# Kernel tuning notes

Hardware: AMD Instinct MI355X
Metric: run time of the kernel (lower is better)

The kernel has to match this reference:

```python
import jax, jax.numpy as jnp
import numpy as np

# ---- static config matching init_kwargs ----
B, H, S, D = 1, 16, 8192, 64
BS = 64                  # block_size (= block_m = block_n here)
NB = S // BS             # 128 query/key blocks
LOCAL = 8                # local window width in blocks

# Block-level sparse pattern: causal, global block 0 + local window of 8 blocks.
_pat = np.zeros((NB, NB), dtype=bool)
for _i in range(NB):
    _pat[_i, 0] = True
    _pat[_i, max(0, _i - LOCAL + 1):_i + 1] = True
MAX_NNZ = int(_pat.sum(1).max())  # 9
_cols = np.zeros((NB, MAX_NNZ), np.int32)
_cmask = np.zeros((NB, MAX_NNZ), bool)
for _i in range(NB):
    _nz = np.nonzero(_pat[_i])[0]
    _cols[_i, :len(_nz)] = _nz
    _cmask[_i, :len(_nz)] = True
COLS = jnp.asarray(_cols)        # [NB, MAX_NNZ] padded column block indices
COLMASK = jnp.asarray(_cmask)    # [NB, MAX_NNZ] validity of padded entries
NEG_INF = jnp.float32(-1e30)


def setup_inputs() -> dict:
    key = jax.random.key(0)
    kq, kk, kv = jax.random.split(key, 3)
    q = jax.random.normal(kq, (B, H, S, D), dtype=jnp.float32)
    k = jax.random.normal(kk, (B, H, S, D), dtype=jnp.float32)
    v = jax.random.normal(kv, (B, H, S, D), dtype=jnp.float32)
    return {"q": q, "k": k, "v": v}


def reference(q, k, v):
    sm_scale = 1.0 / float(np.sqrt(D))
    qb = q.reshape(B, H, NB, BS, D)
    kb = k.reshape(B, H, NB, BS, D)
    vb = v.reshape(B, H, NB, BS, D)
    # gather only the nonzero key/value blocks per query block (honor sparsity)
    kg = kb[:, :, COLS]  # [B,H,NB,MAX_NNZ,BS,D]
    vg = vb[:, :, COLS]  # [B,H,NB,MAX_NNZ,BS,D]
    scores = jnp.einsum('bhimd,bhinjd->bhimnj', qb, kg) * sm_scale  # [B,H,NB,BS,MAX_NNZ,BS]
    # causal + padded-block mask
    q_pos = jnp.arange(NB, dtype=jnp.int32)[:, None] * BS + jnp.arange(BS, dtype=jnp.int32)[None, :]   # [NB,BS]
    k_pos = COLS[:, :, None] * BS + jnp.arange(BS, dtype=jnp.int32)                                     # [NB,MAX_NNZ,BS]
    mask = (k_pos[:, None, :, :] <= q_pos[:, :, None, None]) & COLMASK[:, None, :, None]                # [NB,BS,MAX_NNZ,BS]
    scores = jnp.where(mask, scores, NEG_INF)
    p = jax.nn.softmax(scores.reshape(B, H, NB, BS, MAX_NNZ * BS), axis=-1)
    out = jnp.einsum('bhimn,bhind->bhimd', p, vg.reshape(B, H, NB, MAX_NNZ * BS, D))
    return out.reshape(B, H, S, D)
```

## Files before the change

kernel.cpp:

```cpp
#include <hip/hip_runtime.h>
#include <hip/hip_bf16.h>
#include <string.h>

typedef __attribute__((ext_vector_type(8))) short short8;
typedef __attribute__((ext_vector_type(4))) float floatx4;

#define HH 16
#define SS 8192
#define DD 64
#define NBQ 128
#define NTILE (HH * NBQ)
#define TILE_ELEMS 4096
#define LOG2E 1.44269504088896f
#define WS_NEEDED ((size_t)NTILE * TILE_ELEMS * 2 * 2)

__device__ __forceinline__ unsigned pkbf(float a, float b) {
    __hip_bfloat162 h2 = __float22bfloat162_rn(make_float2(a, b));
    unsigned r;
    memcpy(&r, &h2, 4);
    return r;
}

__device__ __forceinline__ void gload16(const void* g, void* l) {
    __builtin_amdgcn_global_load_lds(
        (const __attribute__((address_space(1))) unsigned int*)g,
        (__attribute__((address_space(3))) unsigned int*)l, 16, 0, 0);
}

__device__ __forceinline__ float red_sum4(float x) {
    x += __shfl_xor(x, 16);
    return x + __shfl_xor(x, 32);
}

__global__ __launch_bounds__(256, 4) void prep_kernel(
        const float* __restrict__ kg, const float* __restrict__ vg,
        unsigned short* __restrict__ kimg, unsigned short* __restrict__ vtimg) {
    __shared__ float lv[64 * 64];
    const int tile = (int)blockIdx.x;
    const int tid = (int)threadIdx.x;
    const float* kb = kg + (size_t)tile * TILE_ELEMS;
    const float* vb = vg + (size_t)tile * TILE_ELEMS;
    unsigned short* ko = kimg + (size_t)tile * TILE_ELEMS;
    unsigned short* vo = vtimg + (size_t)tile * TILE_ELEMS;

    const int row = tid >> 2;
    const int c16 = (tid & 3) * 16;

    {
        const float* src = kb + row * 64 + c16;
        float4 a = ((const float4*)src)[0];
        float4 b = ((const float4*)src)[1];
        float4 c = ((const float4*)src)[2];
        float4 d = ((const float4*)src)[3];
        uint4 lo, hi;
        lo.x = pkbf(a.x, a.y); lo.y = pkbf(a.z, a.w);
        lo.z = pkbf(b.x, b.y); lo.w = pkbf(b.z, b.w);
        hi.x = pkbf(c.x, c.y); hi.y = pkbf(c.z, c.w);
        hi.z = pkbf(d.x, d.y); hi.w = pkbf(d.z, d.w);
        const int sw = (row & 7) << 3;
        *(uint4*)(ko + row * 64 + (c16 ^ sw)) = lo;
        *(uint4*)(ko + row * 64 + ((c16 + 8) ^ sw)) = hi;
    }

    {
        const float4* src = (const float4*)(vb + row * 64 + c16);
        float4* dst = (float4*)(&lv[row * 64 + c16]);
        dst[0] = src[0]; dst[1] = src[1]; dst[2] = src[2]; dst[3] = src[3];
    }
    __syncthreads();
    {
        const int d = row;
        const int kc16 = c16;
        float x[16];
        #pragma unroll
        for (int kk = 0; kk < 16; ++kk) x[kk] = lv[(kc16 + kk) * 64 + d];
        const int sw = (d & 7) << 3;
        const int rot = (d & 15) << 2;
        #pragma unroll
        for (int q4 = 0; q4 < 4; ++q4) {
            uint2 pk;
            pk.x = pkbf(x[4 * q4], x[4 * q4 + 1]);
            pk.y = pkbf(x[4 * q4 + 2], x[4 * q4 + 3]);
            const int c = (((kc16 + 4 * q4) ^ sw) + rot) & 63;
            *(uint2*)(vo + d * 64 + c) = pk;
        }
    }
}

__global__ __launch_bounds__(256, 4) void sparse_attn_kernel(
        const float* __restrict__ qg, const unsigned short* __restrict__ kimg,
        const unsigned short* __restrict__ vtimg, float* __restrict__ og) {
    __shared__ unsigned short lds_k[2][TILE_ELEMS];
    __shared__ unsigned short lds_vt[2][TILE_ELEMS];

    const int bid = (int)blockIdx.x;
    const int work = (bid & 7) * 256 + (bid >> 3);
    const int h = work >> 7;
    const int i = work & (NBQ - 1);
    const int tid = (int)threadIdx.x;
    const int w = tid >> 6;
    const int lane = tid & 63;
    const int lp = lane & 15;
    const int g = lane >> 4;

    const unsigned short* ktiles = kimg + (size_t)h * NBQ * TILE_ELEMS;
    const unsigned short* vtiles = vtimg + (size_t)h * NBQ * TILE_ELEMS;

    short8 qf[2];
    {
        const float sc = 0.125f * LOG2E;
        const float* qrow = qg + ((size_t)h * SS + i * 64 + w * 16 + lp) * DD;
        #pragma unroll
        for (int f = 0; f < 2; ++f) {
            const float* p0 = qrow + f * 32 + 8 * g;
            float4 x = *(const float4*)(p0);
            float4 y = *(const float4*)(p0 + 4);
            union { unsigned u[4]; short8 s; } t_;
            t_.u[0] = pkbf(x.x * sc, x.y * sc);
            t_.u[1] = pkbf(x.z * sc, x.w * sc);
            t_.u[2] = pkbf(y.x * sc, y.y * sc);
            t_.u[3] = pkbf(y.z * sc, y.w * sc);
            qf[f] = t_.s;
        }
    }

    floatx4 acc[4];
    #pragma unroll
    for (int tt = 0; tt < 4; ++tt) acc[tt] = (floatx4)(0.f);
    float lsum = 0.f;

    const int nnz = (i < 8) ? (i + 1) : 9;
    const int lane8 = lane * 8;

    auto stage = [&](int j, int b) {
        const unsigned short* ks = ktiles + (size_t)j * TILE_ELEMS + w * 512 + lane8;
        const unsigned short* vs = vtiles + (size_t)j * TILE_ELEMS + w * 512 + lane8;
        gload16(ks,        &lds_k[b][w * 512]);
        gload16(ks + 2048, &lds_k[b][2048 + w * 512]);
        gload16(vs,        &lds_vt[b][w * 512]);
        gload16(vs + 2048, &lds_vt[b][2048 + w * 512]);
    };

    stage(0, 0);
    __syncthreads();

    const int swl = (lp & 7) << 3;
    int vcol[4];
    #pragma unroll
    for (int r = 0; r < 4; ++r)
        vcol[r] = (((4 * g + 16 * r) ^ swl) + (lp << 2)) & 63;

    for (int t = 0; t < nnz; ++t) {
        const int j = (i < 8) ? t : ((t == 0) ? 0 : (i - 8 + t));
        const int buf = t & 1;

        if (t + 1 < nnz) {
            const int jn = (i < 8) ? (t + 1) : (i - 8 + (t + 1));
            stage(jn, buf ^ 1);
        }

        floatx4 st[4];
        #pragma unroll
        for (int kc = 0; kc < 4; ++kc) st[kc] = (floatx4)(0.f);
        #pragma unroll
        for (int kc = 0; kc < 4; ++kc) {
            const int row = kc * 16 + lp;
            const short8 kf0 = *(const short8*)(&lds_k[buf][row * 64 + ((8 * g) ^ swl)]);
            const short8 kf1 = *(const short8*)(&lds_k[buf][row * 64 + ((32 + 8 * g) ^ swl)]);
            st[kc] = __builtin_amdgcn_mfma_f32_16x16x32_bf16(kf0, qf[0], st[kc], 0, 0, 0);
            st[kc] = __builtin_amdgcn_mfma_f32_16x16x32_bf16(kf1, qf[1], st[kc], 0, 0, 0);
        }

        if (j == i) {
            #pragma unroll
            for (int kc = 0; kc < 4; ++kc) {
                #pragma unroll
                for (int r = 0; r < 4; ++r) {
                    const int key = kc * 16 + 4 * g + r;
                    if (key > w * 16 + lp) st[kc][r] = -1e30f;
                }
            }
        }

        #pragma unroll
        for (int kc = 0; kc < 4; ++kc) {
            #pragma unroll
            for (int r = 0; r < 4; ++r) {
                const float p = exp2f(st[kc][r]);
                st[kc][r] = p;
                lsum += p;
            }
        }

        union { unsigned u[4]; short8 s; } pf0_, pf1_;
        pf0_.u[0] = pkbf(st[0][0], st[0][1]); pf0_.u[1] = pkbf(st[0][2], st[0][3]);
        pf0_.u[2] = pkbf(st[1][0], st[1][1]); pf0_.u[3] = pkbf(st[1][2], st[1][3]);
        pf1_.u[0] = pkbf(st[2][0], st[2][1]); pf1_.u[1] = pkbf(st[2][2], st[2][3]);
        pf1_.u[2] = pkbf(st[3][0], st[3][1]); pf1_.u[3] = pkbf(st[3][2], st[3][3]);
        const short8 pf0 = pf0_.s;
        const short8 pf1 = pf1_.s;

        #pragma unroll
        for (int tt = 0; tt < 4; ++tt) {
            const unsigned short* vr = &lds_vt[buf][(tt * 16 + lp) * 64];
            union { uint2 p[2]; short8 s; } v0_, v1_;
            v0_.p[0] = *(const uint2*)(vr + vcol[0]);
            v0_.p[1] = *(const uint2*)(vr + vcol[1]);
            v1_.p[0] = *(const uint2*)(vr + vcol[2]);
            v1_.p[1] = *(const uint2*)(vr + vcol[3]);
            acc[tt] = __builtin_amdgcn_mfma_f32_16x16x32_bf16(v0_.s, pf0, acc[tt], 0, 0, 0);
            acc[tt] = __builtin_amdgcn_mfma_f32_16x16x32_bf16(v1_.s, pf1, acc[tt], 0, 0, 0);
        }

        if (t + 1 < nnz) __syncthreads();
    }

    const float rn = 1.0f / red_sum4(lsum);
    float* ob = og + ((size_t)h * SS + i * 64 + w * 16 + lp) * DD;
    #pragma unroll
    for (int tt = 0; tt < 4; ++tt) {
        float4 o4;
        o4.x = acc[tt][0] * rn;
        o4.y = acc[tt][1] * rn;
        o4.z = acc[tt][2] * rn;
        o4.w = acc[tt][3] * rn;
        *(float4*)(ob + tt * 16 + 4 * g) = o4;
    }
}

__global__ __launch_bounds__(256, 4) void sparse_attn_fb(
        const float* __restrict__ qg, const float* __restrict__ kg,
        const float* __restrict__ vg, float* __restrict__ og) {
    __shared__ unsigned short lds_k[2][64 * 64];
    __shared__ unsigned short lds_vt[2][64 * 64];
    __shared__ unsigned short lds_p[4][16 * 64];

    const int bid = (int)blockIdx.x;
    const int work = (bid & 7) * 256 + (bid >> 3);
    const int h = work >> 7;
    const int i = work & (NBQ - 1);
    const int tid = (int)threadIdx.x;
    const int w = tid >> 6;
    const int lane = tid & 63;
    const int lp = lane & 15;
    const int g = lane >> 4;

    const float* kh = kg + (size_t)h * SS * DD;
    const float* vh = vg + (size_t)h * SS * DD;

    short8 qf[2];
    {
        const float sc = 0.125f * LOG2E;
        const float* qrow = qg + ((size_t)h * SS + i * 64 + w * 16 + lp) * DD;
        #pragma unroll
        for (int f = 0; f < 2; ++f) {
            const float* p0 = qrow + f * 32 + 8 * g;
            float4 x = *(const float4*)(p0);
            float4 y = *(const float4*)(p0 + 4);
            union { unsigned u[4]; short8 s; } t_;
            t_.u[0] = pkbf(x.x * sc, x.y * sc);
            t_.u[1] = pkbf(x.z * sc, x.w * sc);
            t_.u[2] = pkbf(y.x * sc, y.y * sc);
            t_.u[3] = pkbf(y.z * sc, y.w * sc);
            qf[f] = t_.s;
        }
    }

    floatx4 acc[4];
    #pragma unroll
    for (int tt = 0; tt < 4; ++tt) acc[tt] = (floatx4)(0.f);
    float m = -1e30f;
    float lsum = 0.f;
    const int nnz = (i < 8) ? (i + 1) : 9;

    float4 kreg[4];
    float vreg[16];
    const int krow_sub = tid >> 4;
    const int kc4 = (tid & 15) * 4;

    {
        #pragma unroll
        for (int p = 0; p < 4; ++p)
            kreg[p] = *(const float4*)(kh + (p * 16 + krow_sub) * DD + kc4);
        #pragma unroll
        for (int kk = 0; kk < 16; ++kk)
            vreg[kk] = vh[(w * 16 + kk) * DD + lane];
    }

    const int swl = (lp & 7) << 3;

    for (int t = 0; t < nnz; ++t) {
        const int j = (i < 8) ? t : ((t == 0) ? 0 : (i - 8 + t));
        const int buf = t & 1;

        #pragma unroll
        for (int p = 0; p < 4; ++p) {
            const int row = p * 16 + krow_sub;
            uint2 pk;
            pk.x = pkbf(kreg[p].x, kreg[p].y);
            pk.y = pkbf(kreg[p].z, kreg[p].w);
            *(uint2*)(&lds_k[buf][row * 64 + (kc4 ^ ((row & 7) << 3))]) = pk;
        }
        {
            const int d = lane;
            const int sw = (d & 7) << 3;
            uint4 A, Bv;
            A.x = pkbf(vreg[0], vreg[1]);   A.y = pkbf(vreg[2], vreg[3]);
            A.z = pkbf(vreg[4], vreg[5]);   A.w = pkbf(vreg[6], vreg[7]);
            Bv.x = pkbf(vreg[8], vreg[9]);  Bv.y = pkbf(vreg[10], vreg[11]);
            Bv.z = pkbf(vreg[12], vreg[13]); Bv.w = pkbf(vreg[14], vreg[15]);
            *(uint4*)(&lds_vt[buf][d * 64 + ((w * 16) ^ sw)]) = A;
            *(uint4*)(&lds_vt[buf][d * 64 + ((w * 16 + 8) ^ sw)]) = Bv;
        }

        if (t + 1 < nnz) {
            const int jn = (i < 8) ? (t + 1) : (i - 8 + (t + 1));
            const float* kb = kh + jn * (64 * DD);
            const float* vb = vh + jn * (64 * DD);
            #pragma unroll
            for (int p = 0; p < 4; ++p)
                kreg[p] = *(const float4*)(kb + (p * 16 + krow_sub) * DD + kc4);
            #pragma unroll
            for (int kk = 0; kk < 16; ++kk)
                vreg[kk] = vb[(w * 16 + kk) * DD + lane];
        }

        __syncthreads();

        floatx4 st[4];
        #pragma unroll
        for (int kc = 0; kc < 4; ++kc) st[kc] = (floatx4)(0.f);
        #pragma unroll
        for (int kc = 0; kc < 4; ++kc) {
            const int row = kc * 16 + lp;
            const short8 kf0 = *(const short8*)(&lds_k[buf][row * 64 + ((8 * g) ^ swl)]);
            const short8 kf1 = *(const short8*)(&lds_k[buf][row * 64 + ((32 + 8 * g) ^ swl)]);
            st[kc] = __builtin_amdgcn_mfma_f32_16x16x32_bf16(kf0, qf[0], st[kc], 0, 0, 0);
            st[kc] = __builtin_amdgcn_mfma_f32_16x16x32_bf16(kf1, qf[1], st[kc], 0, 0, 0);
        }

        if (j == i) {
            #pragma unroll
            for (int kc = 0; kc < 4; ++kc) {
                #pragma unroll
                for (int r = 0; r < 4; ++r) {
                    const int key = kc * 16 + 4 * g + r;
                    if (key > w * 16 + lp) st[kc][r] = -1e30f;
                }
            }
        }

        float vmax = -1e30f;
        #pragma unroll
        for (int kc = 0; kc < 4; ++kc) {
            #pragma unroll
            for (int r = 0; r < 4; ++r) vmax = fmaxf(vmax, st[kc][r]);
        }
        vmax = fmaxf(vmax, __shfl_xor(vmax, 16));
        vmax = fmaxf(vmax, __shfl_xor(vmax, 32));
        const float m_new = fmaxf(m, vmax);
        const float alpha = exp2f(m - m_new);
        float psum = 0.f;
        #pragma unroll
        for (int kc = 0; kc < 4; ++kc) {
            #pragma unroll
            for (int r = 0; r < 4; ++r) {
                const float p = exp2f(st[kc][r] - m_new);
                st[kc][r] = p;
                psum += p;
            }
        }
        psum += __shfl_xor(psum, 16);
        psum += __shfl_xor(psum, 32);
        lsum = lsum * alpha + psum;
        m = m_new;
        #pragma unroll
        for (int tt = 0; tt < 4; ++tt) acc[tt] *= alpha;

        unsigned short* pw = lds_p[w];
        #pragma unroll
        for (int kc = 0; kc < 4; ++kc) {
            uint2 pk;
            pk.x = pkbf(st[kc][0], st[kc][1]);
            pk.y = pkbf(st[kc][2], st[kc][3]);
            const int e = lp * 64 + ((kc * 16 + 4 * g) ^ swl);
            *(uint2*)(&pw[e]) = pk;
        }

        const short8 pf0 = *(const short8*)(&pw[lp * 64 + ((8 * g) ^ swl)]);
        const short8 pf1 = *(const short8*)(&pw[lp * 64 + ((32 + 8 * g) ^ swl)]);
        #pragma unroll
        for (int tt = 0; tt < 4; ++tt) {
            const int row = tt * 16 + lp;
            const short8 vf0 = *(const short8*)(&lds_vt[buf][row * 64 + ((8 * g) ^ swl)]);
            const short8 vf1 = *(const short8*)(&lds_vt[buf][row * 64 + ((32 + 8 * g) ^ swl)]);
            acc[tt] = __builtin_amdgcn_mfma_f32_16x16x32_bf16(vf0, pf0, acc[tt], 0, 0, 0);
            acc[tt] = __builtin_amdgcn_mfma_f32_16x16x32_bf16(vf1, pf1, acc[tt], 0, 0, 0);
        }
    }

    const float rn = 1.0f / lsum;
    float* ob = og + ((size_t)h * SS + i * 64 + w * 16 + lp) * DD;
    #pragma unroll
    for (int tt = 0; tt < 4; ++tt) {
        float4 o4;
        o4.x = acc[tt][0] * rn;
        o4.y = acc[tt][1] * rn;
        o4.z = acc[tt][2] * rn;
        o4.w = acc[tt][3] * rn;
        *(float4*)(ob + tt * 16 + 4 * g) = o4;
    }
}

extern "C" void kernel_launch(void* const* d_in, const int* in_sizes, int n_in,
                              void* d_out, int out_size, void* d_ws, size_t ws_size,
                              hipStream_t stream) {
    const float* q = (const float*)d_in[0];
    const float* k = (const float*)d_in[1];
    const float* v = (const float*)d_in[2];
    float* out = (float*)d_out;

    if (ws_size >= WS_NEEDED) {
        unsigned short* kimg = (unsigned short*)d_ws;
        unsigned short* vtimg = kimg + (size_t)NTILE * TILE_ELEMS;
        prep_kernel<<<dim3(NTILE), dim3(256), 0, stream>>>(k, v, kimg, vtimg);
        sparse_attn_kernel<<<dim3(HH * NBQ), dim3(256), 0, stream>>>(q, kimg, vtimg, out);
    } else {
        sparse_attn_fb<<<dim3(HH * NBQ), dim3(256), 0, stream>>>(q, k, v, out);
    }
}
```

Measured before the change: 64.14 us.

## Process two adjacent query blocks per workgroup sharing K/V tile loads

Each workgroup now handles a pair of adjacent query blocks, iterating over the union of their key blocks (global block 0 plus the local window) and reusing each staged K/V tile for both queries. This removes the near-duplicate K/V loads that neighbouring query blocks made into LDS. In exchange the grid is halved to 1024 workgroups, register use roughly doubles for accumulators and scores, and per-tile branches skip MFMAs for blocks outside one query's window.

```diff
diff --git a/kernel.cpp b/kernel.cpp
--- a/kernel.cpp
+++ b/kernel.cpp
@@ -94,6 +94,209 @@
     __shared__ unsigned short lds_vt[2][TILE_ELEMS];
 
     const int bid = (int)blockIdx.x;
+    const int work = (bid & 7) * 128 + (bid >> 3);
+    const int h = work >> 6;
+    const int wi = work & 63;
+    const int i0 = 2 * wi;
+    const int i1 = i0 + 1;
+    const int tid = (int)threadIdx.x;
+    const int w = tid >> 6;
+    const int lane = tid & 63;
+    const int lp = lane & 15;
+    const int g = lane >> 4;
+
+    const unsigned short* ktiles = kimg + (size_t)h * NBQ * TILE_ELEMS;
+    const unsigned short* vtiles = vtimg + (size_t)h * NBQ * TILE_ELEMS;
+
+    short8 qfA[2], qfB[2];
+    {
+        const float sc = 0.125f * LOG2E;
+        const float* qrowA = qg + ((size_t)h * SS + i0 * 64 + w * 16 + lp) * DD;
+        const float* qrowB = qrowA + 64 * DD;
+        #pragma unroll
+        for (int f = 0; f < 2; ++f) {
+            const float* pA = qrowA + f * 32 + 8 * g;
+            float4 xa = *(const float4*)(pA);
+            float4 ya = *(const float4*)(pA + 4);
+            union { unsigned u[4]; short8 s; } tA;
+            tA.u[0] = pkbf(xa.x * sc, xa.y * sc);
+            tA.u[1] = pkbf(xa.z * sc, xa.w * sc);
+            tA.u[2] = pkbf(ya.x * sc, ya.y * sc);
+            tA.u[3] = pkbf(ya.z * sc, ya.w * sc);
+            qfA[f] = tA.s;
+            const float* pB = qrowB + f * 32 + 8 * g;
+            float4 xb = *(const float4*)(pB);
+            float4 yb = *(const float4*)(pB + 4);
+            union { unsigned u[4]; short8 s; } tB;
+            tB.u[0] = pkbf(xb.x * sc, xb.y * sc);
+            tB.u[1] = pkbf(xb.z * sc, xb.w * sc);
+            tB.u[2] = pkbf(yb.x * sc, yb.y * sc);
+            tB.u[3] = pkbf(yb.z * sc, yb.w * sc);
+            qfB[f] = tB.s;
+        }
+    }
+
+    floatx4 accA[4], accB[4];
+    #pragma unroll
+    for (int tt = 0; tt < 4; ++tt) { accA[tt] = (floatx4)(0.f); accB[tt] = (floatx4)(0.f); }
+    float lsumA = 0.f, lsumB = 0.f;
+
+    const int lo = (i0 < 8) ? 1 : (i0 - 7);
+    const int nt = i1 - lo + 2;
+    const int lane8 = lane * 8;
+
+    auto stage = [&](int j, int b) {
+        const unsigned short* ks = ktiles + (size_t)j * TILE_ELEMS + w * 512 + lane8;
+        const unsigned short* vs = vtiles + (size_t)j * TILE_ELEMS + w * 512 + lane8;
+        gload16(ks,        &lds_k[b][w * 512]);
+        gload16(ks + 2048, &lds_k[b][2048 + w * 512]);
+        gload16(vs,        &lds_vt[b][w * 512]);
+        gload16(vs + 2048, &lds_vt[b][2048 + w * 512]);
+    };
+
+    stage(0, 0);
+    __syncthreads();
+
+    const int swl = (lp & 7) << 3;
+    int vcol[4];
+    #pragma unroll
+    for (int r = 0; r < 4; ++r)
+        vcol[r] = (((4 * g + 16 * r) ^ swl) + (lp << 2)) & 63;
+
+    for (int t = 0; t < nt; ++t) {
+        const int j = (t == 0) ? 0 : (lo + t - 1);
+        const int buf = t & 1;
+
+        if (t + 1 < nt) stage(lo + t, buf ^ 1);
+
+        const bool cA = (j == 0) || (j >= i0 - 7 && j <= i0);
+        const bool cB = (j == 0) || (j >= i1 - 7 && j <= i1);
+
+        floatx4 stA[4], stB[4];
+        #pragma unroll
+        for (int kc = 0; kc < 4; ++kc) { stA[kc] = (floatx4)(0.f); stB[kc] = (floatx4)(0.f); }
+        #pragma unroll
+        for (int kc = 0; kc < 4; ++kc) {
+            const int row = kc * 16 + lp;
+            const short8 kf0 = *(const short8*)(&lds_k[buf][row * 64 + ((8 * g) ^ swl)]);
+            const short8 kf1 = *(const short8*)(&lds_k[buf][row * 64 + ((32 + 8 * g) ^ swl)]);
+            if (cA) {
+                stA[kc] = __builtin_amdgcn_mfma_f32_16x16x32_bf16(kf0, qfA[0], stA[kc], 0, 0, 0);
+                stA[kc] = __builtin_amdgcn_mfma_f32_16x16x32_bf16(kf1, qfA[1], stA[kc], 0, 0, 0);
+            }
+            if (cB) {
+                stB[kc] = __builtin_amdgcn_mfma_f32_16x16x32_bf16(kf0, qfB[0], stB[kc], 0, 0, 0);
+                stB[kc] = __builtin_amdgcn_mfma_f32_16x16x32_bf16(kf1, qfB[1], stB[kc], 0, 0, 0);
+            }
+        }
+
+        if (j == i0) {
+            #pragma unroll
+            for (int kc = 0; kc < 4; ++kc)
+                #pragma unroll
+                for (int r = 0; r < 4; ++r)
+                    if (kc * 16 + 4 * g + r > w * 16 + lp) stA[kc][r] = -1e30f;
+        }
+        if (j == i1) {
+            #pragma unroll
+            for (int kc = 0; kc < 4; ++kc)
+                #pragma unroll
+                for (int r = 0; r < 4; ++r)
+                    if (kc * 16 + 4 * g + r > w * 16 + lp) stB[kc][r] = -1e30f;
+        }
+
+        if (cA) {
+            #pragma unroll
+            for (int kc = 0; kc < 4; ++kc)
+                #pragma unroll
+                for (int r = 0; r < 4; ++r) {
+                    const float p = exp2f(stA[kc][r]);
+                    stA[kc][r] = p;
+                    lsumA += p;
+                }
+        }
+        if (cB) {
+            #pragma unroll
+            for (int kc = 0; kc < 4; ++kc)
+                #pragma unroll
+                for (int r = 0; r < 4; ++r) {
+                    const float p = exp2f(stB[kc][r]);
+                    stB[kc][r] = p;
+                    lsumB += p;
+                }
+        }
+
+        short8 pfA0, pfA1, pfB0, pfB1;
+        if (cA) {
+            union { unsigned u[4]; short8 s; } p0_, p1_;
+            p0_.u[0] = pkbf(stA[0][0], stA[0][1]); p0_.u[1] = pkbf(stA[0][2], stA[0][3]);
+            p0_.u[2] = pkbf(stA[1][0], stA[1][1]); p0_.u[3] = pkbf(stA[1][2], stA[1][3]);
+            p1_.u[0] = pkbf(stA[2][0], stA[2][1]); p1_.u[1] = pkbf(stA[2][2], stA[2][3]);
+            p1_.u[2] = pkbf(stA[3][0], stA[3][1]); p1_.u[3] = pkbf(stA[3][2], stA[3][3]);
+            pfA0 = p0_.s; pfA1 = p1_.s;
+        }
+        if (cB) {
+            union { unsigned u[4]; short8 s; } p0_, p1_;
+            p0_.u[0] = pkbf(stB[0][0], stB[0][1]); p0_.u[1] = pkbf(stB[0][2], stB[0][3]);
+            p0_.u[2] = pkbf(stB[1][0], stB[1][1]); p0_.u[3] = pkbf(stB[1][2], stB[1][3]);
+            p1_.u[0] = pkbf(stB[2][0], stB[2][1]); p1_.u[1] = pkbf(stB[2][2], stB[2][3]);
+            p1_.u[2] = pkbf(stB[3][0], stB[3][1]); p1_.u[3] = pkbf(stB[3][2], stB[3][3]);
+            pfB0 = p0_.s; pfB1 = p1_.s;
+        }
+
+        #pragma unroll
+        for (int tt = 0; tt < 4; ++tt) {
+            const unsigned short* vr = &lds_vt[buf][(tt * 16 + lp) * 64];
+            union { uint2 p[2]; short8 s; } v0_, v1_;
+            v0_.p[0] = *(const uint2*)(vr + vcol[0]);
+            v0_.p[1] = *(const uint2*)(vr + vcol[1]);
+            v1_.p[0] = *(const uint2*)(vr + vcol[2]);
+            v1_.p[1] = *(const uint2*)(vr + vcol[3]);
+            if (cA) {
+                accA[tt] = __builtin_amdgcn_mfma_f32_16x16x32_bf16(v0_.s, pfA0, accA[tt], 0, 0, 0);
+                accA[tt] = __builtin_amdgcn_mfma_f32_16x16x32_bf16(v1_.s, pfA1, accA[tt], 0, 0, 0);
+            }
+            if (cB) {
+                accB[tt] = __builtin_amdgcn_mfma_f32_16x16x32_bf16(v0_.s, pfB0, accB[tt], 0, 0, 0);
+                accB[tt] = __builtin_amdgcn_mfma_f32_16x16x32_bf16(v1_.s, pfB1, accB[tt], 0, 0, 0);
+            }
+        }
+
+        if (t + 1 < nt) __syncthreads();
+    }
+
+    {
+        const float rn = 1.0f / red_sum4(lsumA);
+        float* ob = og + ((size_t)h * SS + i0 * 64 + w * 16 + lp) * DD;
+        #pragma unroll
+        for (int tt = 0; tt < 4; ++tt) {
+            float4 o4;
+            o4.x = accA[tt][0] * rn; o4.y = accA[tt][1] * rn;
+            o4.z = accA[tt][2] * rn; o4.w = accA[tt][3] * rn;
+            *(float4*)(ob + tt * 16 + 4 * g) = o4;
+        }
+    }
+    {
+        const float rn = 1.0f / red_sum4(lsumB);
+        float* ob = og + ((size_t)h * SS + i1 * 64 + w * 16 + lp) * DD;
+        #pragma unroll
+        for (int tt = 0; tt < 4; ++tt) {
+            float4 o4;
+            o4.x = accB[tt][0] * rn; o4.y = accB[tt][1] * rn;
+            o4.z = accB[tt][2] * rn; o4.w = accB[tt][3] * rn;
+            *(float4*)(ob + tt * 16 + 4 * g) = o4;
+        }
+    }
+}
+
+__global__ __launch_bounds__(256, 4) void sparse_attn_fb(
+        const float* __restrict__ qg, const float* __restrict__ kg,
+        const float* __restrict__ vg, float* __restrict__ og) {
+    __shared__ unsigned short lds_k[2][64 * 64];
+    __shared__ unsigned short lds_vt[2][64 * 64];
+    __shared__ unsigned short lds_p[4][16 * 64];
+
+    const int bid = (int)blockIdx.x;
     const int work = (bid & 7) * 256 + (bid >> 3);
     const int h = work >> 7;
     const int i = work & (NBQ - 1);
@@ -103,8 +306,8 @@
     const int lp = lane & 15;
     const int g = lane >> 4;
 
-    const unsigned short* ktiles = kimg + (size_t)h * NBQ * TILE_ELEMS;
-    const unsigned short* vtiles = vtimg + (size_t)h * NBQ * TILE_ELEMS;
+    const float* kh = kg + (size_t)h * SS * DD;
+    const float* vh = vg + (size_t)h * SS * DD;
 
     short8 qf[2];
     {
@@ -127,148 +330,6 @@
     floatx4 acc[4];
     #pragma unroll
     for (int tt = 0; tt < 4; ++tt) acc[tt] = (floatx4)(0.f);
-    float lsum = 0.f;
-
-    const int nnz = (i < 8) ? (i + 1) : 9;
-    const int lane8 = lane * 8;
-
-    auto stage = [&](int j, int b) {
-        const unsigned short* ks = ktiles + (size_t)j * TILE_ELEMS + w * 512 + lane8;
-        const unsigned short* vs = vtiles + (size_t)j * TILE_ELEMS + w * 512 + lane8;
-        gload16(ks,        &lds_k[b][w * 512]);
-        gload16(ks + 2048, &lds_k[b][2048 + w * 512]);
-        gload16(vs,        &lds_vt[b][w * 512]);
-        gload16(vs + 2048, &lds_vt[b][2048 + w * 512]);
-    };
-
-    stage(0, 0);
-    __syncthreads();
-
-    const int swl = (lp & 7) << 3;
-    int vcol[4];
-    #pragma unroll
-    for (int r = 0; r < 4; ++r)
-        vcol[r] = (((4 * g + 16 * r) ^ swl) + (lp << 2)) & 63;
-
-    for (int t = 0; t < nnz; ++t) {
-        const int j = (i < 8) ? t : ((t == 0) ? 0 : (i - 8 + t));
-        const int buf = t & 1;
-
-        if (t + 1 < nnz) {
-            const int jn = (i < 8) ? (t + 1) : (i - 8 + (t + 1));
-            stage(jn, buf ^ 1);
-        }
-
-        floatx4 st[4];
-        #pragma unroll
-        for (int kc = 0; kc < 4; ++kc) st[kc] = (floatx4)(0.f);
-        #pragma unroll
-        for (int kc = 0; kc < 4; ++kc) {
-            const int row = kc * 16 + lp;
-            const short8 kf0 = *(const short8*)(&lds_k[buf][row * 64 + ((8 * g) ^ swl)]);
-            const short8 kf1 = *(const short8*)(&lds_k[buf][row * 64 + ((32 + 8 * g) ^ swl)]);
-            st[kc] = __builtin_amdgcn_mfma_f32_16x16x32_bf16(kf0, qf[0], st[kc], 0, 0, 0);
-            st[kc] = __builtin_amdgcn_mfma_f32_16x16x32_bf16(kf1, qf[1], st[kc], 0, 0, 0);
-        }
-
-        if (j == i) {
-            #pragma unroll
-            for (int kc = 0; kc < 4; ++kc) {
-                #pragma unroll
-                for (int r = 0; r < 4; ++r) {
-                    const int key = kc * 16 + 4 * g + r;
-                    if (key > w * 16 + lp) st[kc][r] = -1e30f;
-                }
-            }
-        }
-
-        #pragma unroll
-        for (int kc = 0; kc < 4; ++kc) {
-            #pragma unroll
-            for (int r = 0; r < 4; ++r) {
-                const float p = exp2f(st[kc][r]);
-                st[kc][r] = p;
-                lsum += p;
-            }
-        }
-
-        union { unsigned u[4]; short8 s; } pf0_, pf1_;
-        pf0_.u[0] = pkbf(st[0][0], st[0][1]); pf0_.u[1] = pkbf(st[0][2], st[0][3]);
-        pf0_.u[2] = pkbf(st[1][0], st[1][1]); pf0_.u[3] = pkbf(st[1][2], st[1][3]);
-        pf1_.u[0] = pkbf(st[2][0], st[2][1]); pf1_.u[1] = pkbf(st[2][2], st[2][3]);
-        pf1_.u[2] = pkbf(st[3][0], st[3][1]); pf1_.u[3] = pkbf(st[3][2], st[3][3]);
-        const short8 pf0 = pf0_.s;
-        const short8 pf1 = pf1_.s;
-
-        #pragma unroll
-        for (int tt = 0; tt < 4; ++tt) {
-            const unsigned short* vr = &lds_vt[buf][(tt * 16 + lp) * 64];
-            union { uint2 p[2]; short8 s; } v0_, v1_;
-            v0_.p[0] = *(const uint2*)(vr + vcol[0]);
-            v0_.p[1] = *(const uint2*)(vr + vcol[1]);
-            v1_.p[0] = *(const uint2*)(vr + vcol[2]);
-            v1_.p[1] = *(const uint2*)(vr + vcol[3]);
-            acc[tt] = __builtin_amdgcn_mfma_f32_16x16x32_bf16(v0_.s, pf0, acc[tt], 0, 0, 0);
-            acc[tt] = __builtin_amdgcn_mfma_f32_16x16x32_bf16(v1_.s, pf1, acc[tt], 0, 0, 0);
-        }
-
-        if (t + 1 < nnz) __syncthreads();
-    }
-
-    const float rn = 1.0f / red_sum4(lsum);
-    float* ob = og + ((size_t)h * SS + i * 64 + w * 16 + lp) * DD;
-    #pragma unroll
-    for (int tt = 0; tt < 4; ++tt) {
-        float4 o4;
-        o4.x = acc[tt][0] * rn;
-        o4.y = acc[tt][1] * rn;
-        o4.z = acc[tt][2] * rn;
-        o4.w = acc[tt][3] * rn;
-        *(float4*)(ob + tt * 16 + 4 * g) = o4;
-    }
-}
-
-__global__ __launch_bounds__(256, 4) void sparse_attn_fb(
-        const float* __restrict__ qg, const float* __restrict__ kg,
-        const float* __restrict__ vg, float* __restrict__ og) {
-    __shared__ unsigned short lds_k[2][64 * 64];
-    __shared__ unsigned short lds_vt[2][64 * 64];
-    __shared__ unsigned short lds_p[4][16 * 64];
-
-    const int bid = (int)blockIdx.x;
-    const int work = (bid & 7) * 256 + (bid >> 3);
-    const int h = work >> 7;
-    const int i = work & (NBQ - 1);
-    const int tid = (int)threadIdx.x;
-    const int w = tid >> 6;
-    const int lane = tid & 63;
-    const int lp = lane & 15;
-    const int g = lane >> 4;
-
-    const float* kh = kg + (size_t)h * SS * DD;
-    const float* vh = vg + (size_t)h * SS * DD;
-
-    short8 qf[2];
-    {
-        const float sc = 0.125f * LOG2E;
-        const float* qrow = qg + ((size_t)h * SS + i * 64 + w * 16 + lp) * DD;
-        #pragma unroll
-        for (int f = 0; f < 2; ++f) {
-            const float* p0 = qrow + f * 32 + 8 * g;
-            float4 x = *(const float4*)(p0);
-            float4 y = *(const float4*)(p0 + 4);
-            union { unsigned u[4]; short8 s; } t_;
-            t_.u[0] = pkbf(x.x * sc, x.y * sc);
-            t_.u[1] = pkbf(x.z * sc, x.w * sc);
-            t_.u[2] = pkbf(y.x * sc, y.y * sc);
-            t_.u[3] = pkbf(y.z * sc, y.w * sc);
-            qf[f] = t_.s;
-        }
-    }
-
-    floatx4 acc[4];
-    #pragma unroll
-    for (int tt = 0; tt < 4; ++tt) acc[tt] = (floatx4)(0.f);
     float m = -1e30f;
     float lsum = 0.f;
     const int nnz = (i < 8) ? (i + 1) : 9;
@@ -424,7 +485,7 @@
         unsigned short* kimg = (unsigned short*)d_ws;
         unsigned short* vtimg = kimg + (size_t)NTILE * TILE_ELEMS;
         prep_kernel<<<dim3(NTILE), dim3(256), 0, stream>>>(k, v, kimg, vtimg);
-        sparse_attn_kernel<<<dim3(HH * NBQ), dim3(256), 0, stream>>>(q, kimg, vtimg, out);
+        sparse_attn_kernel<<<dim3(HH * 64), dim3(256), 0, stream>>>(q, kimg, vtimg, out);
     } else {
         sparse_attn_fb<<<dim3(HH * NBQ), dim3(256), 0, stream>>>(q, k, v, out);
     }
```

New measurement: 120.1 us. +87.2%, slower.

## Process two adjacent query blocks per workgroup to share staged K/V tiles

Applied to the files above, without the earlier changes.

Each 512-thread workgroup now handles two consecutive query blocks, with four waves per block. The union of their key/value tiles (global block plus the combined local window) is staged once into LDS and shared. Each half skips tiles outside its own window. This roughly halves K/V global-to-LDS traffic per query block, at the cost of one extra loop iteration, more barrier participants, and fewer workgroups in the grid.

```diff
diff --git a/kernel.cpp b/kernel.cpp
--- a/kernel.cpp
+++ b/kernel.cpp
@@ -87,18 +87,22 @@
     }
 }
 
-__global__ __launch_bounds__(256, 4) void sparse_attn_kernel(
+__global__ __launch_bounds__(512, 4) void sparse_attn_kernel(
         const float* __restrict__ qg, const unsigned short* __restrict__ kimg,
         const unsigned short* __restrict__ vtimg, float* __restrict__ og) {
     __shared__ unsigned short lds_k[2][TILE_ELEMS];
     __shared__ unsigned short lds_vt[2][TILE_ELEMS];
 
     const int bid = (int)blockIdx.x;
-    const int work = (bid & 7) * 256 + (bid >> 3);
-    const int h = work >> 7;
-    const int i = work & (NBQ - 1);
+    const int work = (bid & 7) * 128 + (bid >> 3);
+    const int h = work >> 6;
+    const int wi = work & 63;
+    const int i0 = 2 * wi;
     const int tid = (int)threadIdx.x;
-    const int w = tid >> 6;
+    const int half = tid >> 8;
+    const int im = i0 + half;
+    const int w = (tid >> 6) & 3;
+    const int w8 = tid >> 6;
     const int lane = tid & 63;
     const int lp = lane & 15;
     const int g = lane >> 4;
@@ -109,7 +113,7 @@
     short8 qf[2];
     {
         const float sc = 0.125f * LOG2E;
-        const float* qrow = qg + ((size_t)h * SS + i * 64 + w * 16 + lp) * DD;
+        const float* qrow = qg + ((size_t)h * SS + im * 64 + w * 16 + lp) * DD;
         #pragma unroll
         for (int f = 0; f < 2; ++f) {
             const float* p0 = qrow + f * 32 + 8 * g;
@@ -129,16 +133,14 @@
     for (int tt = 0; tt < 4; ++tt) acc[tt] = (floatx4)(0.f);
     float lsum = 0.f;
 
-    const int nnz = (i < 8) ? (i + 1) : 9;
-    const int lane8 = lane * 8;
+    const int lo = (i0 < 8) ? 1 : (i0 - 7);
+    const int nt = (i0 + 1) - lo + 2;
 
     auto stage = [&](int j, int b) {
-        const unsigned short* ks = ktiles + (size_t)j * TILE_ELEMS + w * 512 + lane8;
-        const unsigned short* vs = vtiles + (size_t)j * TILE_ELEMS + w * 512 + lane8;
-        gload16(ks,        &lds_k[b][w * 512]);
-        gload16(ks + 2048, &lds_k[b][2048 + w * 512]);
-        gload16(vs,        &lds_vt[b][w * 512]);
-        gload16(vs + 2048, &lds_vt[b][2048 + w * 512]);
+        const unsigned short* ks = ktiles + (size_t)j * TILE_ELEMS + w8 * 512 + lane * 8;
+        const unsigned short* vs = vtiles + (size_t)j * TILE_ELEMS + w8 * 512 + lane * 8;
+        gload16(ks, &lds_k[b][w8 * 512]);
+        gload16(vs, &lds_vt[b][w8 * 512]);
     };
 
     stage(0, 0);
@@ -150,73 +152,69 @@
     for (int r = 0; r < 4; ++r)
         vcol[r] = (((4 * g + 16 * r) ^ swl) + (lp << 2)) & 63;
 
-    for (int t = 0; t < nnz; ++t) {
-        const int j = (i < 8) ? t : ((t == 0) ? 0 : (i - 8 + t));
+    for (int t = 0; t < nt; ++t) {
+        const int j = (t == 0) ? 0 : (lo + t - 1);
         const int buf = t & 1;
 
-        if (t + 1 < nnz) {
-            const int jn = (i < 8) ? (t + 1) : (i - 8 + (t + 1));
-            stage(jn, buf ^ 1);
-        }
-
-        floatx4 st[4];
-        #pragma unroll
-        for (int kc = 0; kc < 4; ++kc) st[kc] = (floatx4)(0.f);
-        #pragma unroll
-        for (int kc = 0; kc < 4; ++kc) {
-            const int row = kc * 16 + lp;
-            const short8 kf0 = *(const short8*)(&lds_k[buf][row * 64 + ((8 * g) ^ swl)]);
-            const short8 kf1 = *(const short8*)(&lds_k[buf][row * 64 + ((32 + 8 * g) ^ swl)]);
-            st[kc] = __builtin_amdgcn_mfma_f32_16x16x32_bf16(kf0, qf[0], st[kc], 0, 0, 0);
-            st[kc] = __builtin_amdgcn_mfma_f32_16x16x32_bf16(kf1, qf[1], st[kc], 0, 0, 0);
-        }
-
-        if (j == i) {
+        if (t + 1 < nt) stage(lo + t, buf ^ 1);
+
+        const bool c = (j == 0) || (j >= im - 7 && j <= im);
+        if (c) {
+            floatx4 st[4];
+            #pragma unroll
+            for (int kc = 0; kc < 4; ++kc) st[kc] = (floatx4)(0.f);
             #pragma unroll
             for (int kc = 0; kc < 4; ++kc) {
+                const int row = kc * 16 + lp;
+                const short8 kf0 = *(const short8*)(&lds_k[buf][row * 64 + ((8 * g) ^ swl)]);
+                const short8 kf1 = *(const short8*)(&lds_k[buf][row * 64 + ((32 + 8 * g) ^ swl)]);
+                st[kc] = __builtin_amdgcn_mfma_f32_16x16x32_bf16(kf0, qf[0], st[kc], 0, 0, 0);
+                st[kc] = __builtin_amdgcn_mfma_f32_16x16x32_bf16(kf1, qf[1], st[kc], 0, 0, 0);
+            }
+
+            if (j == im) {
+                #pragma unroll
+                for (int kc = 0; kc < 4; ++kc)
+                    #pragma unroll
+                    for (int r = 0; r < 4; ++r)
+                        if (kc * 16 + 4 * g + r > w * 16 + lp) st[kc][r] = -1e30f;
+            }
+
+            #pragma unroll
+            for (int kc = 0; kc < 4; ++kc)
                 #pragma unroll
                 for (int r = 0; r < 4; ++r) {
-                    const int key = kc * 16 + 4 * g + r;
-                    if (key > w * 16 + lp) st[kc][r] = -1e30f;
+                    const float p = exp2f(st[kc][r]);
+                    st[kc][r] = p;
+                    lsum += p;
                 }
+
+            union { unsigned u[4]; short8 s; } pf0_, pf1_;
+            pf0_.u[0] = pkbf(st[0][0], st[0][1]); pf0_.u[1] = pkbf(st[0][2], st[0][3]);
+            pf0_.u[2] = pkbf(st[1][0], st[1][1]); pf0_.u[3] = pkbf(st[1][2], st[1][3]);
+            pf1_.u[0] = pkbf(st[2][0], st[2][1]); pf1_.u[1] = pkbf(st[2][2], st[2][3]);
+            pf1_.u[2] = pkbf(st[3][0], st[3][1]); pf1_.u[3] = pkbf(st[3][2], st[3][3]);
+            const short8 pf0 = pf0_.s;
+            const short8 pf1 = pf1_.s;
+
+            #pragma unroll
+            for (int tt = 0; tt < 4; ++tt) {
+                const unsigned short* vr = &lds_vt[buf][(tt * 16 + lp) * 64];
+                union { uint2 p[2]; short8 s; } v0_, v1_;
+                v0_.p[0] = *(const uint2*)(vr + vcol[0]);
+                v0_.p[1] = *(const uint2*)(vr + vcol[1]);
+                v1_.p[0] = *(const uint2*)(vr + vcol[2]);
+                v1_.p[1] = *(const uint2*)(vr + vcol[3]);
+                acc[tt] = __builtin_amdgcn_mfma_f32_16x16x32_bf16(v0_.s, pf0, acc[tt], 0, 0, 0);
+                acc[tt] = __builtin_amdgcn_mfma_f32_16x16x32_bf16(v1_.s, pf1, acc[tt], 0, 0, 0);
             }
         }
 
-        #pragma unroll
-        for (int kc = 0; kc < 4; ++kc) {
-            #pragma unroll
-            for (int r = 0; r < 4; ++r) {
-                const float p = exp2f(st[kc][r]);
-                st[kc][r] = p;
-                lsum += p;
-            }
-        }
-
-        union { unsigned u[4]; short8 s; } pf0_, pf1_;
-        pf0_.u[0] = pkbf(st[0][0], st[0][1]); pf0_.u[1] = pkbf(st[0][2], st[0][3]);
-        pf0_.u[2] = pkbf(st[1][0], st[1][1]); pf0_.u[3] = pkbf(st[1][2], st[1][3]);
-        pf1_.u[0] = pkbf(st[2][0], st[2][1]); pf1_.u[1] = pkbf(st[2][2], st[2][3]);
-        pf1_.u[2] = pkbf(st[3][0], st[3][1]); pf1_.u[3] = pkbf(st[3][2], st[3][3]);
-        const short8 pf0 = pf0_.s;
-        const short8 pf1 = pf1_.s;
-
-        #pragma unroll
-        for (int tt = 0; tt < 4; ++tt) {
-            const unsigned short* vr = &lds_vt[buf][(tt * 16 + lp) * 64];
-            union { uint2 p[2]; short8 s; } v0_, v1_;
-            v0_.p[0] = *(const uint2*)(vr + vcol[0]);
-            v0_.p[1] = *(const uint2*)(vr + vcol[1]);
-            v1_.p[0] = *(const uint2*)(vr + vcol[2]);
-            v1_.p[1] = *(const uint2*)(vr + vcol[3]);
-            acc[tt] = __builtin_amdgcn_mfma_f32_16x16x32_bf16(v0_.s, pf0, acc[tt], 0, 0, 0);
-            acc[tt] = __builtin_amdgcn_mfma_f32_16x16x32_bf16(v1_.s, pf1, acc[tt], 0, 0, 0);
-        }
-
-        if (t + 1 < nnz) __syncthreads();
+        if (t + 1 < nt) __syncthreads();
     }
 
     const float rn = 1.0f / red_sum4(lsum);
-    float* ob = og + ((size_t)h * SS + i * 64 + w * 16 + lp) * DD;
+    float* ob = og + ((size_t)h * SS + im * 64 + w * 16 + lp) * DD;
     #pragma unroll
     for (int tt = 0; tt < 4; ++tt) {
         float4 o4;
@@ -424,7 +422,7 @@
         unsigned short* kimg = (unsigned short*)d_ws;
         unsigned short* vtimg = kimg + (size_t)NTILE * TILE_ELEMS;
         prep_kernel<<<dim3(NTILE), dim3(256), 0, stream>>>(k, v, kimg, vtimg);
-        sparse_attn_kernel<<<dim3(HH * NBQ), dim3(256), 0, stream>>>(q, kimg, vtimg, out);
+        sparse_attn_kernel<<<dim3(HH * 64), dim3(512), 0, stream>>>(q, kimg, vtimg, out);
     } else {
         sparse_attn_fb<<<dim3(HH * NBQ), dim3(256), 0, stream>>>(q, k, v, out);
     }
```

Result: slower. 65.71 us (+2.4%).

## Pre-lay K/V into MFMA fragment order and load directly from global

Applied to the files above, without the earlier changes.

The prep kernel now writes K and transposed V tiles in per-lane MFMA fragment order, so each lane reads its 16-byte operand pairs straight from global memory. The attention kernel drops LDS staging, double buffering and the per-step barriers, and raises the launch-bounds occupancy hint to 6. It also switches exp2f to the native exp2 builtin. The cost is that overlap of loads with compute now depends on the compiler and occupancy rather than explicit prefetch, and the uncoalesced fragment reads lean on L2 for the reuse across neighbouring query blocks.

```diff
diff --git a/kernel.cpp b/kernel.cpp
--- a/kernel.cpp
+++ b/kernel.cpp
@@ -21,10 +21,12 @@
     return r;
 }
 
-__device__ __forceinline__ void gload16(const void* g, void* l) {
-    __builtin_amdgcn_global_load_lds(
-        (const __attribute__((address_space(1))) unsigned int*)g,
-        (__attribute__((address_space(3))) unsigned int*)l, 16, 0, 0);
+__device__ __forceinline__ float fexp2(float x) {
+#if __has_builtin(__builtin_amdgcn_exp2f)
+    return __builtin_amdgcn_exp2f(x);
+#else
+    return exp2f(x);
+#endif
 }
 
 __device__ __forceinline__ float red_sum4(float x) {
@@ -43,56 +45,54 @@
     unsigned short* ko = kimg + (size_t)tile * TILE_ELEMS;
     unsigned short* vo = vtimg + (size_t)tile * TILE_ELEMS;
 
-    const int row = tid >> 2;
-    const int c16 = (tid & 3) * 16;
-
-    {
-        const float* src = kb + row * 64 + c16;
-        float4 a = ((const float4*)src)[0];
-        float4 b = ((const float4*)src)[1];
-        float4 c = ((const float4*)src)[2];
-        float4 d = ((const float4*)src)[3];
+    const int r = tid >> 2;
+    const int g = tid & 3;
+
+    {
+        const float* s0 = kb + r * 64 + 8 * g;
+        const float* s1 = kb + r * 64 + 32 + 8 * g;
+        float4 a = ((const float4*)s0)[0];
+        float4 b = ((const float4*)s0)[1];
+        float4 c = ((const float4*)s1)[0];
+        float4 d = ((const float4*)s1)[1];
         uint4 lo, hi;
         lo.x = pkbf(a.x, a.y); lo.y = pkbf(a.z, a.w);
         lo.z = pkbf(b.x, b.y); lo.w = pkbf(b.z, b.w);
         hi.x = pkbf(c.x, c.y); hi.y = pkbf(c.z, c.w);
         hi.z = pkbf(d.x, d.y); hi.w = pkbf(d.z, d.w);
-        const int sw = (row & 7) << 3;
-        *(uint4*)(ko + row * 64 + (c16 ^ sw)) = lo;
-        *(uint4*)(ko + row * 64 + ((c16 + 8) ^ sw)) = hi;
-    }
-
-    {
-        const float4* src = (const float4*)(vb + row * 64 + c16);
-        float4* dst = (float4*)(&lv[row * 64 + c16]);
+        unsigned short* dst = ko + (r * 4 + g) * 16;
+        *(uint4*)(dst) = lo;
+        *(uint4*)(dst + 8) = hi;
+    }
+
+    {
+        const float4* src = (const float4*)(vb + r * 64 + g * 16);
+        float4* dst = (float4*)(&lv[r * 64 + g * 16]);
         dst[0] = src[0]; dst[1] = src[1]; dst[2] = src[2]; dst[3] = src[3];
     }
     __syncthreads();
     {
-        const int d = row;
-        const int kc16 = c16;
+        const int d = r;
         float x[16];
         #pragma unroll
-        for (int kk = 0; kk < 16; ++kk) x[kk] = lv[(kc16 + kk) * 64 + d];
-        const int sw = (d & 7) << 3;
-        const int rot = (d & 15) << 2;
-        #pragma unroll
-        for (int q4 = 0; q4 < 4; ++q4) {
-            uint2 pk;
-            pk.x = pkbf(x[4 * q4], x[4 * q4 + 1]);
-            pk.y = pkbf(x[4 * q4 + 2], x[4 * q4 + 3]);
-            const int c = (((kc16 + 4 * q4) ^ sw) + rot) & 63;
-            *(uint2*)(vo + d * 64 + c) = pk;
-        }
-    }
-}
-
-__global__ __launch_bounds__(256, 4) void sparse_attn_kernel(
+        for (int q4 = 0; q4 < 4; ++q4)
+            #pragma unroll
+            for (int cc = 0; cc < 4; ++cc)
+                x[q4 * 4 + cc] = lv[(q4 * 16 + 4 * g + cc) * 64 + d];
+        uint4 lo, hi;
+        lo.x = pkbf(x[0], x[1]);   lo.y = pkbf(x[2], x[3]);
+        lo.z = pkbf(x[4], x[5]);   lo.w = pkbf(x[6], x[7]);
+        hi.x = pkbf(x[8], x[9]);   hi.y = pkbf(x[10], x[11]);
+        hi.z = pkbf(x[12], x[13]); hi.w = pkbf(x[14], x[15]);
+        unsigned short* dst = vo + (d * 4 + g) * 16;
+        *(uint4*)(dst) = lo;
+        *(uint4*)(dst + 8) = hi;
+    }
+}
+
+__global__ __launch_bounds__(256, 6) void sparse_attn_kernel(
         const float* __restrict__ qg, const unsigned short* __restrict__ kimg,
         const unsigned short* __restrict__ vtimg, float* __restrict__ og) {
-    __shared__ unsigned short lds_k[2][TILE_ELEMS];
-    __shared__ unsigned short lds_vt[2][TILE_ELEMS];
-
     const int bid = (int)blockIdx.x;
     const int work = (bid & 7) * 256 + (bid >> 3);
     const int h = work >> 7;
@@ -103,8 +103,9 @@
     const int lp = lane & 15;
     const int g = lane >> 4;
 
-    const unsigned short* ktiles = kimg + (size_t)h * NBQ * TILE_ELEMS;
-    const unsigned short* vtiles = vtimg + (size_t)h * NBQ * TILE_ELEMS;
+    const int loff = (lp * 4 + g) * 16;
+    const unsigned short* ktiles = kimg + (size_t)h * NBQ * TILE_ELEMS + loff;
+    const unsigned short* vtiles = vtimg + (size_t)h * NBQ * TILE_ELEMS + loff;
 
     short8 qf[2];
     {
@@ -130,67 +131,39 @@
     float lsum = 0.f;
 
     const int nnz = (i < 8) ? (i + 1) : 9;
-    const int lane8 = lane * 8;
-
-    auto stage = [&](int j, int b) {
-        const unsigned short* ks = ktiles + (size_t)j * TILE_ELEMS + w * 512 + lane8;
-        const unsigned short* vs = vtiles + (size_t)j * TILE_ELEMS + w * 512 + lane8;
-        gload16(ks,        &lds_k[b][w * 512]);
-        gload16(ks + 2048, &lds_k[b][2048 + w * 512]);
-        gload16(vs,        &lds_vt[b][w * 512]);
-        gload16(vs + 2048, &lds_vt[b][2048 + w * 512]);
-    };
-
-    stage(0, 0);
-    __syncthreads();
-
-    const int swl = (lp & 7) << 3;
-    int vcol[4];
-    #pragma unroll
-    for (int r = 0; r < 4; ++r)
-        vcol[r] = (((4 * g + 16 * r) ^ swl) + (lp << 2)) & 63;
 
     for (int t = 0; t < nnz; ++t) {
         const int j = (i < 8) ? t : ((t == 0) ? 0 : (i - 8 + t));
-        const int buf = t & 1;
-
-        if (t + 1 < nnz) {
-            const int jn = (i < 8) ? (t + 1) : (i - 8 + (t + 1));
-            stage(jn, buf ^ 1);
-        }
+        const unsigned short* kt = ktiles + (size_t)j * TILE_ELEMS;
+        const unsigned short* vt = vtiles + (size_t)j * TILE_ELEMS;
 
         floatx4 st[4];
         #pragma unroll
         for (int kc = 0; kc < 4; ++kc) st[kc] = (floatx4)(0.f);
         #pragma unroll
         for (int kc = 0; kc < 4; ++kc) {
-            const int row = kc * 16 + lp;
-            const short8 kf0 = *(const short8*)(&lds_k[buf][row * 64 + ((8 * g) ^ swl)]);
-            const short8 kf1 = *(const short8*)(&lds_k[buf][row * 64 + ((32 + 8 * g) ^ swl)]);
+            const short8 kf0 = *(const short8*)(kt + kc * 1024);
+            const short8 kf1 = *(const short8*)(kt + kc * 1024 + 8);
             st[kc] = __builtin_amdgcn_mfma_f32_16x16x32_bf16(kf0, qf[0], st[kc], 0, 0, 0);
             st[kc] = __builtin_amdgcn_mfma_f32_16x16x32_bf16(kf1, qf[1], st[kc], 0, 0, 0);
         }
 
         if (j == i) {
             #pragma unroll
-            for (int kc = 0; kc < 4; ++kc) {
+            for (int kc = 0; kc < 4; ++kc)
                 #pragma unroll
-                for (int r = 0; r < 4; ++r) {
-                    const int key = kc * 16 + 4 * g + r;
-                    if (key > w * 16 + lp) st[kc][r] = -1e30f;
-                }
-            }
-        }
-
-        #pragma unroll
-        for (int kc = 0; kc < 4; ++kc) {
+                for (int r = 0; r < 4; ++r)
+                    if (kc * 16 + 4 * g + r > w * 16 + lp) st[kc][r] = -1e30f;
+        }
+
+        #pragma unroll
+        for (int kc = 0; kc < 4; ++kc)
             #pragma unroll
             for (int r = 0; r < 4; ++r) {
-                const float p = exp2f(st[kc][r]);
+                const float p = fexp2(st[kc][r]);
                 st[kc][r] = p;
                 lsum += p;
             }
-        }
 
         union { unsigned u[4]; short8 s; } pf0_, pf1_;
         pf0_.u[0] = pkbf(st[0][0], st[0][1]); pf0_.u[1] = pkbf(st[0][2], st[0][3]);
@@ -202,17 +175,11 @@
 
         #pragma unroll
         for (int tt = 0; tt < 4; ++tt) {
-            const unsigned short* vr = &lds_vt[buf][(tt * 16 + lp) * 64];
-            union { uint2 p[2]; short8 s; } v0_, v1_;
-            v0_.p[0] = *(const uint2*)(vr + vcol[0]);
-            v0_.p[1] = *(const uint2*)(vr + vcol[1]);
-            v1_.p[0] = *(const uint2*)(vr + vcol[2]);
-            v1_.p[1] = *(const uint2*)(vr + vcol[3]);
-            acc[tt] = __builtin_amdgcn_mfma_f32_16x16x32_bf16(v0_.s, pf0, acc[tt], 0, 0, 0);
-            acc[tt] = __builtin_amdgcn_mfma_f32_16x16x32_bf16(v1_.s, pf1, acc[tt], 0, 0, 0);
-        }
-
-        if (t + 1 < nnz) __syncthreads();
+            const short8 vf0 = *(const short8*)(vt + tt * 1024);
+            const short8 vf1 = *(const short8*)(vt + tt * 1024 + 8);
+            acc[tt] = __builtin_amdgcn_mfma_f32_16x16x32_bf16(vf0, pf0, acc[tt], 0, 0, 0);
+            acc[tt] = __builtin_amdgcn_mfma_f32_16x16x32_bf16(vf1, pf1, acc[tt], 0, 0, 0);
+        }
     }
 
     const float rn = 1.0f / red_sum4(lsum);
```

New measurement: 180.9 us. 182% more time.
